# Kernel tuning notes

Hardware: AMD Instinct MI355X
Metric: run time of the kernel (lower is better)

Reference implementation:

```python
import jax, jax.numpy as jnp
import numpy as np

NMS_RADIUS = 2.0   # cfgs.NMS_radius (meters)
EPS = 1e-6         # torch nn.PairwiseDistance default eps (added to the diff)
M = 16384          # number of keypoint candidates
SCENE = 100.0      # scene extent in meters


def setup_inputs() -> dict:
    key = jax.random.key(0)
    k1, k2 = jax.random.split(key)
    nodes = jax.random.uniform(k1, (M, 3), dtype=jnp.float32) * SCENE
    overlap_score = jax.random.normal(k2, (M,), dtype=jnp.float32)
    return {"nodes": nodes, "overlap_score": overlap_score}


def _greedy_nms(nodes, radius):
    """Sequential greedy NMS: keep node i iff its distance to every
    already-kept node exceeds radius. Faithful to the torch loop:
    (dis > radius).sum() == n_kept  <=>  all kept dists > radius."""
    n = nodes.shape[0]

    def body(i, mask):
        # torch nn.PairwiseDistance computes ||x1 - x2 + eps||_2
        d = jnp.linalg.norm(nodes[i] - nodes + EPS, axis=-1)  # [n]
        keep = jnp.all(jnp.where(mask, d > radius, True))
        return mask.at[i].set(keep)

    mask0 = jnp.zeros(n, dtype=bool).at[0].set(True)
    return jax.lax.fori_loop(1, n, body, mask0)


def reference(nodes, overlap_score):
    # sort by overlap score descending, run greedy NMS, unsort the mask
    order = jnp.argsort(-overlap_score)
    mask_sorted = _greedy_nms(nodes[order], NMS_RADIUS)
    mask = jnp.zeros_like(mask_sorted).at[order].set(mask_sorted)
    nms_length = mask.sum(dtype=jnp.int32)[None]
    return mask, nms_length
```

## Files before the change

### kernel.cpp

```cpp
#include <hip/hip_runtime.h>


#define M_PTS    16384
#define RADIUS   2.0f
#define EPS_D    1e-6f
#define GRID_N   25
#define NCELLS   (GRID_N * GRID_N * GRID_N)
#define CELL_CAP 12
#define K_NBR    12
#define EPT      5
#define ACT_PAD  (EPT * 1024)
#define CELLS_PB (GRID_N * GRID_N)
#define LIST_PB  (CELLS_PB * CELL_CAP)


__device__ __forceinline__ int cell_of(float v) {
  int c = (int)(v * 0.25f);
  return c < 0 ? 0 : (c > GRID_N - 1 ? GRID_N - 1 : c);
}

__device__ __forceinline__ bool edge_test(float4 pi, float4 pj, int j, int i) {
  bool earlier = (pj.w > pi.w) || ((pj.w == pi.w) && (j < i));
  if (!earlier) return false;
  float ddx = __fadd_rn(__fsub_rn(pi.x, pj.x), EPS_D);
  float ddy = __fadd_rn(__fsub_rn(pi.y, pj.y), EPS_D);
  float ddz = __fadd_rn(__fsub_rn(pi.z, pj.z), EPS_D);
  float d2 = __fadd_rn(__fadd_rn(__fmul_rn(ddx, ddx), __fmul_rn(ddy, ddy)),
                       __fmul_rn(ddz, ddz));
  return !(__fsqrt_rn(d2) > RADIUS);
}

__global__ __launch_bounds__(1024) void bin25(
    const float* __restrict__ nodes, const float* __restrict__ score,
    float4* __restrict__ pts, int* __restrict__ cell_cnt,
    unsigned short* __restrict__ cell_list) {
  __shared__ int ccnt[CELLS_PB];
  __shared__ unsigned short clist[LIST_PB];
  const int tid = threadIdx.x;
  const int b   = blockIdx.x;
  if (tid < CELLS_PB) ccnt[tid] = 0;
  __syncthreads();

  for (int i = tid; i < M_PTS; i += 1024) {
    float x = nodes[3 * i + 0];
    if (cell_of(x) != b) continue;
    float y = nodes[3 * i + 1];
    float z = nodes[3 * i + 2];
    float s = score[i];
    pts[i] = make_float4(x, y, z, s);
    int lc = cell_of(y) * GRID_N + cell_of(z);
    int pos = atomicAdd(&ccnt[lc], 1);
    if (pos < CELL_CAP) clist[lc * CELL_CAP + pos] = (unsigned short)i;
  }
  __syncthreads();

  if (tid < CELLS_PB) {
    int v = ccnt[tid];
    cell_cnt[b * CELLS_PB + tid] = v > CELL_CAP ? CELL_CAP : v;
  }
  for (int e = tid; e < LIST_PB; e += 1024)
    cell_list[b * LIST_PB + e] = clist[e];
}

__global__ __launch_bounds__(256) void wscan(
    const float4* __restrict__ pts, const int* __restrict__ cell_cnt,
    const unsigned short* __restrict__ cell_list,
    int* __restrict__ cnt, unsigned short* __restrict__ nbr) {
  const int tid  = threadIdx.x;
  const int lane = tid & 63;
  const int d    = lane & 31;
  const int half = lane >> 5;
  const int gwave = (blockIdx.x * 256 + tid) >> 6;
  const int i = gwave * 2 + half;

  const float4 pi = pts[i];
  int n = 0, cid = 0, m = 0, firstj = 0;
  if (d < 27) {
    int cx = cell_of(pi.x) + d / 9 - 1;
    int cy = cell_of(pi.y) + (d / 3) % 3 - 1;
    int cz = cell_of(pi.z) + d % 3 - 1;
    if (cx >= 0 && cx < GRID_N && cy >= 0 && cy < GRID_N &&
        cz >= 0 && cz < GRID_N) {
      cid = (cx * GRID_N + cy) * GRID_N + cz;
      m = cell_cnt[cid];
      for (int s = 0; s < m; ++s) {
        int j = cell_list[cid * CELL_CAP + s];
        if (edge_test(pi, pts[j], j, i)) { if (!n) firstj = j; ++n; }
      }
    }
  }
  int x = n;
#pragma unroll
  for (int off = 1; off < 32; off <<= 1) {
    int y = __shfl_up(x, off, 32);
    if (d >= off) x += y;
  }
  int excl = x - n;
  int tot = __shfl(x, 31, 32);
  if (n == 1) {
    if (excl < K_NBR) nbr[i * K_NBR + excl] = (unsigned short)firstj;
  } else if (n > 1) {
    int pos = excl;
    for (int s = 0; s < m && pos < K_NBR; ++s) {
      int j = cell_list[cid * CELL_CAP + s];
      if (edge_test(pi, pts[j], j, i)) {
        nbr[i * K_NBR + pos] = (unsigned short)j;
        ++pos;
      }
    }
  }
  if (d == 0) cnt[i] = tot > K_NBR ? K_NBR : tot;
}

__global__ __launch_bounds__(1024) void solve_kernel(
    const int* __restrict__ cnt, const unsigned short* __restrict__ nbr,
    int* __restrict__ out, int out_size) {
  __shared__ unsigned char mask_[M_PTS];
  __shared__ unsigned int act[ACT_PAD];
  __shared__ int act_n, total;
  volatile unsigned char* mask = mask_;

  const int tid = threadIdx.x;
  const int lane = tid & 63;
  if (tid == 0) { act_n = 0; total = 0; }
  for (int a = tid; a < ACT_PAD; a += 1024) act[a] = 0u;
  __syncthreads();

  for (int k = tid; k < M_PTS; k += 1024) {
    mask_[k] = 1;
    int c = cnt[k];
    if (c > K_NBR) c = K_NBR;
    unsigned long long b = __ballot(c > 0);
    int wcnt = __popcll(b);
    int wbase = 0;
    if (lane == 0 && wcnt) wbase = atomicAdd(&act_n, wcnt);
    wbase = __shfl(wbase, 0, 64);
    if (c > 0) {
      int pos = wbase + __popcll(b & ((1ull << lane) - 1ull));
      if (pos < ACT_PAD) act[pos] = (unsigned)k | ((unsigned)c << 16);
    }
  }
  __syncthreads();
  const int na = act_n;
  const bool ok = (na <= ACT_PAD);

  unsigned ae[EPT];
  unsigned short r0[EPT], r1[EPT], r2[EPT];
#pragma unroll
  for (int e = 0; e < EPT; ++e) {
    unsigned v = act[tid + e * 1024];
    ae[e] = v;
    int k = (int)(v & 0xFFFFu);
    int c = (int)(v >> 16);
    const unsigned short* row = nbr + (size_t)k * K_NBR;
    r0[e] = (c > 0) ? row[0] : (unsigned short)0;
    r1[e] = (c > 1) ? row[1] : (unsigned short)0;
    r2[e] = (c > 2) ? row[2] : (unsigned short)0;
  }
  __syncthreads();

  if (ok) {
    for (int it = 0; it < 96; ++it) {
      int any = 0;
      int m0[EPT];
#pragma unroll
      for (int e = 0; e < EPT; ++e) m0[e] = (int)mask[r0[e]];
#pragma unroll
      for (int e = 0; e < EPT; ++e) {
        unsigned v = ae[e];
        int c = (int)(v >> 16);
        if (!c) continue;
        int k = (int)(v & 0xFFFFu);
        int kp = m0[e] ^ 1;
        if (c > 1) kp &= (int)mask[r1[e]] ^ 1;
        if (c > 2) kp &= (int)mask[r2[e]] ^ 1;
        if (c > 3) {
          const unsigned short* row = nbr + (size_t)k * K_NBR;
          for (int t = 3; t < c; ++t) kp &= (int)mask[row[t]] ^ 1;
        }
        if (kp != (int)mask[k]) { mask[k] = (unsigned char)kp; any = 1; }
      }
      if (__syncthreads_count(any) == 0) break;
    }
  } else {
    __shared__ int changed;
    for (int it = 0; it < 512; ++it) {
      if (tid == 0) changed = 0;
      __syncthreads();
      int any = 0;
      for (int k = tid; k < M_PTS; k += 1024) {
        int c = cnt[k]; if (c > K_NBR) c = K_NBR;
        if (!c) continue;
        int kp = 1;
        for (int t = 0; t < c; ++t) kp &= (int)mask[nbr[k * K_NBR + t]] ^ 1;
        if (kp != (int)mask[k]) { mask_[k] = (unsigned char)kp; any = 1; }
      }
      if (any) changed = 1;
      __syncthreads();
      if (!changed) break;
    }
  }
  __syncthreads();

  int ks = 0;
  for (int k = tid; k < M_PTS; k += 1024) {
    int m = (int)mask_[k];
    out[k] = m;
    ks += m;
  }
#pragma unroll
  for (int off = 32; off > 0; off >>= 1) ks += __shfl_down(ks, off, 64);
  if (lane == 0) atomicAdd(&total, ks);
  __syncthreads();
  if (tid == 0) out[out_size - 1] = total;
}

extern "C" void kernel_launch(void* const* d_in, const int* in_sizes, int n_in,
                              void* d_out, int out_size, void* d_ws, size_t ws_size,
                              hipStream_t stream) {
  const float* nodes = (const float*)d_in[0];
  const float* score = (const float*)d_in[1];
  int* out = (int*)d_out;

  char* ws = (char*)d_ws;
  float4* pts = (float4*)ws;
  int* cell_cnt = (int*)(ws + 262144);
  int* cnt = (int*)(ws + 327680);
  unsigned short* cell_list = (unsigned short*)(ws + 393216);
  unsigned short* nbr = (unsigned short*)(ws + 770048);

  bin25<<<GRID_N, 1024, 0, stream>>>(nodes, score, pts, cell_cnt, cell_list);
  wscan<<<2048, 256, 0, stream>>>(pts, cell_cnt, cell_list, cnt, nbr);
  solve_kernel<<<1, 1024, 0, stream>>>(cnt, nbr, out, out_size);
}
```

Baseline: 42.70 us.

## Replace iterative Jacobi NMS solve with per-thread memoized DFS over earlier-neighbor DAG

The single-block solve stage no longer iterates the whole active set with barriers until convergence. Each thread now resolves nodes by depth-first evaluation over their earlier neighbors, memoizing results in shared memory, with the first two neighbor indices packed into a per-node word. This removes repeated barrier-separated sweeps. Concurrent threads may redundantly recompute shared subchains, and an overflow of the 32-entry stack falls back to the old iterative sweep.

New measurement: 84.34 us. 1.98x slower.

```diff
diff --git a/kernel.cpp b/kernel.cpp
--- a/kernel.cpp
+++ b/kernel.cpp
@@ -8,8 +8,6 @@
 #define NCELLS   (GRID_N * GRID_N * GRID_N)
 #define CELL_CAP 12
 #define K_NBR    12
-#define EPT      5
-#define ACT_PAD  (EPT * 1024)
 #define CELLS_PB (GRID_N * GRID_N)
 #define LIST_PB  (CELLS_PB * CELL_CAP)
 
@@ -112,99 +110,97 @@
   if (d == 0) cnt[i] = tot > K_NBR ? K_NBR : tot;
 }
 
-__global__ __launch_bounds__(1024) void solve_kernel(
+__global__ __launch_bounds__(1024) void solve_dfs(
     const int* __restrict__ cnt, const unsigned short* __restrict__ nbr,
     int* __restrict__ out, int out_size) {
-  __shared__ unsigned char mask_[M_PTS];
-  __shared__ unsigned int act[ACT_PAD];
-  __shared__ int act_n, total;
-  volatile unsigned char* mask = mask_;
+  __shared__ unsigned int pack[M_PTS];
+  __shared__ unsigned char memo_[M_PTS];
+  __shared__ int total;
+  volatile unsigned char* memo = memo_;
 
   const int tid = threadIdx.x;
   const int lane = tid & 63;
-  if (tid == 0) { act_n = 0; total = 0; }
-  for (int a = tid; a < ACT_PAD; a += 1024) act[a] = 0u;
-  __syncthreads();
+  if (tid == 0) total = 0;
 
   for (int k = tid; k < M_PTS; k += 1024) {
-    mask_[k] = 1;
     int c = cnt[k];
     if (c > K_NBR) c = K_NBR;
-    unsigned long long b = __ballot(c > 0);
-    int wcnt = __popcll(b);
-    int wbase = 0;
-    if (lane == 0 && wcnt) wbase = atomicAdd(&act_n, wcnt);
-    wbase = __shfl(wbase, 0, 64);
+    unsigned p = (unsigned)c;
     if (c > 0) {
-      int pos = wbase + __popcll(b & ((1ull << lane) - 1ull));
-      if (pos < ACT_PAD) act[pos] = (unsigned)k | ((unsigned)c << 16);
-    }
-  }
-  __syncthreads();
-  const int na = act_n;
-  const bool ok = (na <= ACT_PAD);
-
-  unsigned ae[EPT];
-  unsigned short r0[EPT], r1[EPT], r2[EPT];
-#pragma unroll
-  for (int e = 0; e < EPT; ++e) {
-    unsigned v = act[tid + e * 1024];
-    ae[e] = v;
-    int k = (int)(v & 0xFFFFu);
-    int c = (int)(v >> 16);
-    const unsigned short* row = nbr + (size_t)k * K_NBR;
-    r0[e] = (c > 0) ? row[0] : (unsigned short)0;
-    r1[e] = (c > 1) ? row[1] : (unsigned short)0;
-    r2[e] = (c > 2) ? row[2] : (unsigned short)0;
-  }
-  __syncthreads();
-
-  if (ok) {
+      unsigned w = *(const unsigned int*)(nbr + (size_t)k * K_NBR);
+      p |= (w & 0x3FFFu) << 4;
+      if (c > 1) p |= ((w >> 16) & 0x3FFFu) << 18;
+      memo_[k] = 0xFF;
+    } else {
+      memo_[k] = 1;
+    }
+    pack[k] = p;
+  }
+  __syncthreads();
+
+  int ovf = 0;
+  for (int k0 = tid; k0 < M_PTS; k0 += 1024) {
+    if (memo[k0] != 0xFF) continue;
+    unsigned short st[32];
+    int sp = 0;
+    st[sp++] = (unsigned short)k0;
+    while (sp > 0) {
+      int u = st[sp - 1];
+      if (memo[u] != 0xFF) { --sp; continue; }
+      unsigned p = pack[u];
+      int c = (int)(p & 15u);
+      int kp = 1, all = 1;
+      int cc = c < 2 ? c : 2;
+      for (int t = 0; t < cc; ++t) {
+        int j = (t == 0) ? (int)((p >> 4) & 0x3FFFu) : (int)((p >> 18) & 0x3FFFu);
+        int mv = memo[j];
+        if (mv == 0xFF) {
+          if (sp < 32) st[sp++] = (unsigned short)j; else ovf = 1;
+          all = 0;
+        } else kp &= mv ^ 1;
+      }
+      if (c > 2) {
+        const unsigned short* row = nbr + (size_t)u * K_NBR;
+        for (int t = 2; t < c; ++t) {
+          int j = row[t];
+          int mv = memo[j];
+          if (mv == 0xFF) {
+            if (sp < 32) st[sp++] = (unsigned short)j; else ovf = 1;
+            all = 0;
+          } else kp &= mv ^ 1;
+        }
+      }
+      if (ovf) break;
+      if (all) { memo[u] = (unsigned char)kp; --sp; }
+    }
+    if (ovf) break;
+  }
+
+  if (__syncthreads_count(ovf) != 0) {
+    for (int k = tid; k < M_PTS; k += 1024)
+      if (memo_[k] == 0xFF) memo_[k] = 1;
+    __syncthreads();
     for (int it = 0; it < 96; ++it) {
       int any = 0;
-      int m0[EPT];
-#pragma unroll
-      for (int e = 0; e < EPT; ++e) m0[e] = (int)mask[r0[e]];
-#pragma unroll
-      for (int e = 0; e < EPT; ++e) {
-        unsigned v = ae[e];
-        int c = (int)(v >> 16);
+      for (int k = tid; k < M_PTS; k += 1024) {
+        unsigned p = pack[k];
+        int c = (int)(p & 15u);
         if (!c) continue;
-        int k = (int)(v & 0xFFFFu);
-        int kp = m0[e] ^ 1;
-        if (c > 1) kp &= (int)mask[r1[e]] ^ 1;
-        if (c > 2) kp &= (int)mask[r2[e]] ^ 1;
-        if (c > 3) {
+        int kp = (int)memo[(p >> 4) & 0x3FFFu] ^ 1;
+        if (c > 1) kp &= (int)memo[(p >> 18) & 0x3FFFu] ^ 1;
+        if (c > 2) {
           const unsigned short* row = nbr + (size_t)k * K_NBR;
-          for (int t = 3; t < c; ++t) kp &= (int)mask[row[t]] ^ 1;
+          for (int t = 2; t < c; ++t) kp &= (int)memo[row[t]] ^ 1;
         }
-        if (kp != (int)mask[k]) { mask[k] = (unsigned char)kp; any = 1; }
+        if (kp != (int)memo[k]) { memo[k] = (unsigned char)kp; any = 1; }
       }
       if (__syncthreads_count(any) == 0) break;
     }
-  } else {
-    __shared__ int changed;
-    for (int it = 0; it < 512; ++it) {
-      if (tid == 0) changed = 0;
-      __syncthreads();
-      int any = 0;
-      for (int k = tid; k < M_PTS; k += 1024) {
-        int c = cnt[k]; if (c > K_NBR) c = K_NBR;
-        if (!c) continue;
-        int kp = 1;
-        for (int t = 0; t < c; ++t) kp &= (int)mask[nbr[k * K_NBR + t]] ^ 1;
-        if (kp != (int)mask[k]) { mask_[k] = (unsigned char)kp; any = 1; }
-      }
-      if (any) changed = 1;
-      __syncthreads();
-      if (!changed) break;
-    }
-  }
-  __syncthreads();
+  }
 
   int ks = 0;
   for (int k = tid; k < M_PTS; k += 1024) {
-    int m = (int)mask_[k];
+    int m = (int)memo_[k];
     out[k] = m;
     ks += m;
   }
@@ -231,5 +227,5 @@
 
   bin25<<<GRID_N, 1024, 0, stream>>>(nodes, score, pts, cell_cnt, cell_list);
   wscan<<<2048, 256, 0, stream>>>(pts, cell_cnt, cell_list, cnt, nbr);
-  solve_kernel<<<1, 1024, 0, stream>>>(cnt, nbr, out, out_size);
-}
+  solve_dfs<<<1, 1024, 0, stream>>>(cnt, nbr, out, out_size);
+}
```

## Resolve NMS via chain pointer-jumping and branch-point fixpoint instead of full Jacobi iteration

Applied to the files above, without the earlier changes.

Rewrites the single-block solve kernel. Nodes with one earlier neighbour are resolved by walking their dependency chain and tracking parity. Only nodes with two or more neighbours (branch points, at most three unresolved targets) go through a small iterative fixpoint, and deferred chain nodes are filled in afterwards. This is meant to replace the many-iteration, full-mask relaxation with far fewer barriers. When any capacity or shape assumption is violated it falls back to the old global iteration, which adds risk and extra code paths.

After: 44.73 us. 4.7% more time.

```diff
diff --git a/kernel.cpp b/kernel.cpp
--- a/kernel.cpp
+++ b/kernel.cpp
@@ -8,10 +8,11 @@
 #define NCELLS   (GRID_N * GRID_N * GRID_N)
 #define CELL_CAP 12
 #define K_NBR    12
-#define EPT      5
-#define ACT_PAD  (EPT * 1024)
 #define CELLS_PB (GRID_N * GRID_N)
 #define LIST_PB  (CELLS_PB * CELL_CAP)
+#define SENT     M_PTS
+#define BB_CAP   1024
+#define DFR_CAP  2048
 
 
 __device__ __forceinline__ int cell_of(float v) {
@@ -112,99 +113,165 @@
   if (d == 0) cnt[i] = tot > K_NBR ? K_NBR : tot;
 }
 
-__global__ __launch_bounds__(1024) void solve_kernel(
+__global__ __launch_bounds__(1024) void solve_cc(
     const int* __restrict__ cnt, const unsigned short* __restrict__ nbr,
     int* __restrict__ out, int out_size) {
-  __shared__ unsigned char mask_[M_PTS];
-  __shared__ unsigned int act[ACT_PAD];
-  __shared__ int act_n, total;
-  volatile unsigned char* mask = mask_;
+  __shared__ unsigned int pack[M_PTS];
+  __shared__ unsigned char val[M_PTS + 4];
+  __shared__ unsigned short bb[BB_CAP];
+  __shared__ unsigned int dfr[DFR_CAP];
+  __shared__ int nbb, ndfr, total, fail;
 
   const int tid = threadIdx.x;
   const int lane = tid & 63;
-  if (tid == 0) { act_n = 0; total = 0; }
-  for (int a = tid; a < ACT_PAD; a += 1024) act[a] = 0u;
-  __syncthreads();
+  if (tid == 0) { nbb = 0; ndfr = 0; total = 0; fail = 0; }
 
   for (int k = tid; k < M_PTS; k += 1024) {
-    mask_[k] = 1;
-    int c = cnt[k];
-    if (c > K_NBR) c = K_NBR;
-    unsigned long long b = __ballot(c > 0);
-    int wcnt = __popcll(b);
-    int wbase = 0;
-    if (lane == 0 && wcnt) wbase = atomicAdd(&act_n, wcnt);
-    wbase = __shfl(wbase, 0, 64);
-    if (c > 0) {
-      int pos = wbase + __popcll(b & ((1ull << lane) - 1ull));
-      if (pos < ACT_PAD) act[pos] = (unsigned)k | ((unsigned)c << 16);
-    }
-  }
-  __syncthreads();
-  const int na = act_n;
-  const bool ok = (na <= ACT_PAD);
-
-  unsigned ae[EPT];
-  unsigned short r0[EPT], r1[EPT], r2[EPT];
-#pragma unroll
-  for (int e = 0; e < EPT; ++e) {
-    unsigned v = act[tid + e * 1024];
-    ae[e] = v;
-    int k = (int)(v & 0xFFFFu);
-    int c = (int)(v >> 16);
-    const unsigned short* row = nbr + (size_t)k * K_NBR;
-    r0[e] = (c > 0) ? row[0] : (unsigned short)0;
-    r1[e] = (c > 1) ? row[1] : (unsigned short)0;
-    r2[e] = (c > 2) ? row[2] : (unsigned short)0;
-  }
-  __syncthreads();
-
-  if (ok) {
-    for (int it = 0; it < 96; ++it) {
-      int any = 0;
-      int m0[EPT];
-#pragma unroll
-      for (int e = 0; e < EPT; ++e) m0[e] = (int)mask[r0[e]];
-#pragma unroll
-      for (int e = 0; e < EPT; ++e) {
-        unsigned v = ae[e];
-        int c = (int)(v >> 16);
-        if (!c) continue;
-        int k = (int)(v & 0xFFFFu);
-        int kp = m0[e] ^ 1;
-        if (c > 1) kp &= (int)mask[r1[e]] ^ 1;
-        if (c > 2) kp &= (int)mask[r2[e]] ^ 1;
-        if (c > 3) {
-          const unsigned short* row = nbr + (size_t)k * K_NBR;
-          for (int t = 3; t < c; ++t) kp &= (int)mask[row[t]] ^ 1;
+    int c = cnt[k]; if (c > K_NBR) c = K_NBR;
+    unsigned r0 = (c > 0) ? (unsigned)nbr[(size_t)k * K_NBR] : 0u;
+    pack[k] = (unsigned)c | (r0 << 4);
+    val[k] = (c == 0) ? 1 : 0xFF;
+  }
+  if (tid == 0) val[SENT] = 0;
+  __syncthreads();
+
+  for (int k = tid; k < M_PTS; k += 1024) {
+    int c = (int)(pack[k] & 15u);
+    bool isbb = (c >= 2);
+    unsigned long long bal = __ballot(isbb);
+    if (bal) {
+      int wcnt = __popcll(bal);
+      int wbase = 0;
+      if (lane == 0) wbase = atomicAdd(&nbb, wcnt);
+      wbase = __shfl(wbase, 0, 64);
+      if (isbb) {
+        int pos = wbase + __popcll(bal & ((1ull << lane) - 1ull));
+        if (pos < BB_CAP) bb[pos] = (unsigned short)k; else fail = 1;
+      }
+    }
+    if (c == 1) {
+      int j = (int)(pack[k] >> 4);
+      int parity = 1, steps = 0;
+      while ((pack[j] & 15u) == 1u && steps < 64) {
+        j = (int)(pack[j] >> 4); parity ^= 1; ++steps;
+      }
+      unsigned cj = pack[j] & 15u;
+      if (cj == 0u) val[k] = (unsigned char)(1 ^ parity);
+      else if (cj == 1u) fail = 1;
+      else {
+        int pos = atomicAdd(&ndfr, 1);
+        if (pos < DFR_CAP)
+          dfr[pos] = (unsigned)k | ((unsigned)j << 14) | ((unsigned)parity << 28);
+        else fail = 1;
+      }
+    }
+  }
+  __syncthreads();
+
+  const int NBB = nbb < BB_CAP ? nbb : BB_CAP;
+  const int NDFR = ndfr < DFR_CAP ? ndfr : DFR_CAP;
+
+  int ownk = -1, resolved = 1;
+  unsigned short tt0 = SENT, tt1 = SENT, tt2 = SENT;
+  int q0 = 1, q1 = 1, q2 = 1;
+  if (!fail && tid < NBB) {
+    ownk = bb[tid];
+    int c = (int)(pack[ownk] & 15u);
+    const unsigned short* row = nbr + (size_t)ownk * K_NBR;
+    int dead = 0, nu = 0, lfail = 0;
+    for (int t = 0; t < c; ++t) {
+      int p = row[t];
+      int v = val[p];
+      if (v != 0xFF) {
+        if (v == 1) dead = 1;
+      } else {
+        int cp = (int)(pack[p] & 15u);
+        int tgt = p, par = 0;
+        if (cp == 1) {
+          int j = (int)(pack[p] >> 4);
+          par = 1;
+          int steps = 0;
+          while ((pack[j] & 15u) == 1u && steps < 64) {
+            j = (int)(pack[j] >> 4); par ^= 1; ++steps;
+          }
+          unsigned cj = pack[j] & 15u;
+          if (cj == 1u) { lfail = 1; tgt = -1; }
+          else if (cj == 0u) { if (par == 0) dead = 1; tgt = -1; }
+          else tgt = j;
         }
-        if (kp != (int)mask[k]) { mask[k] = (unsigned char)kp; any = 1; }
-      }
-      if (__syncthreads_count(any) == 0) break;
-    }
-  } else {
+        if (tgt >= 0) {
+          int q = par ^ 1;
+          if (nu == 0)      { tt0 = (unsigned short)tgt; q0 = q; }
+          else if (nu == 1) { tt1 = (unsigned short)tgt; q1 = q; }
+          else if (nu == 2) { tt2 = (unsigned short)tgt; q2 = q; }
+          else lfail = 1;
+          ++nu;
+        }
+      }
+    }
+    if (lfail) fail = 1;
+    else if (dead) val[ownk] = 0;
+    else if (nu == 0) val[ownk] = 1;
+    else resolved = 0;
+  }
+  __syncthreads();
+
+  if (!fail) {
+    for (int it = 0; it < 64; ++it) {
+      int unres = 0;
+      if (!resolved) {
+        int v0 = val[tt0], v1 = val[tt1], v2 = val[tt2];
+        int kn0 = (v0 != 0xFF), kn1 = (v1 != 0xFF), kn2 = (v2 != 0xFF);
+        int t0 = v0 ^ q0, t1 = v1 ^ q1, t2 = v2 ^ q2;
+        if ((kn0 && t0 == 0) || (kn1 && t1 == 0) || (kn2 && t2 == 0)) {
+          val[ownk] = 0; resolved = 1;
+        } else if (kn0 && kn1 && kn2) {
+          val[ownk] = (unsigned char)(t0 & t1 & t2); resolved = 1;
+        } else unres = 1;
+      }
+      if (__syncthreads_count(unres) == 0) break;
+    }
+    if (!resolved) fail = 1;
+  }
+  __syncthreads();
+
+  if (!fail) {
+    for (int idx = tid; idx < NDFR; idx += 1024) {
+      unsigned e = dfr[idx];
+      int k = (int)(e & 0x3FFFu);
+      int t = (int)((e >> 14) & 0x3FFFu);
+      int par = (int)(e >> 28);
+      val[k] = (unsigned char)(val[t] ^ par);
+    }
+  }
+  __syncthreads();
+
+  if (fail) {
+    for (int k = tid; k < M_PTS; k += 1024) val[k] = 1;
+    __syncthreads();
     __shared__ int changed;
     for (int it = 0; it < 512; ++it) {
       if (tid == 0) changed = 0;
       __syncthreads();
       int any = 0;
       for (int k = tid; k < M_PTS; k += 1024) {
-        int c = cnt[k]; if (c > K_NBR) c = K_NBR;
+        int c = (int)(pack[k] & 15u);
         if (!c) continue;
         int kp = 1;
-        for (int t = 0; t < c; ++t) kp &= (int)mask[nbr[k * K_NBR + t]] ^ 1;
-        if (kp != (int)mask[k]) { mask_[k] = (unsigned char)kp; any = 1; }
+        const unsigned short* row = nbr + (size_t)k * K_NBR;
+        for (int t = 0; t < c; ++t) kp &= (int)val[row[t]] ^ 1;
+        if (kp != (int)val[k]) { val[k] = (unsigned char)kp; any = 1; }
       }
       if (any) changed = 1;
       __syncthreads();
       if (!changed) break;
     }
-  }
-  __syncthreads();
+    __syncthreads();
+  }
 
   int ks = 0;
   for (int k = tid; k < M_PTS; k += 1024) {
-    int m = (int)mask_[k];
+    int m = (int)val[k];
     out[k] = m;
     ks += m;
   }
@@ -231,5 +298,5 @@
 
   bin25<<<GRID_N, 1024, 0, stream>>>(nodes, score, pts, cell_cnt, cell_list);
   wscan<<<2048, 256, 0, stream>>>(pts, cell_cnt, cell_list, cnt, nbr);
-  solve_kernel<<<1, 1024, 0, stream>>>(cnt, nbr, out, out_size);
-}
+  solve_cc<<<1, 1024, 0, stream>>>(cnt, nbr, out, out_size);
+}
```
